# Performance work log

Measured on AMD Instinct MI355X. Metric: run time of the kernel, lower is better.

Reference implementation:

```python
import jax, jax.numpy as jnp
import numpy as np

B, N, F_IN, F_OUT = 64, 1024, 256, 64


def setup_inputs() -> dict:
    key = jax.random.key(0)
    k1, k2, k3, k4 = jax.random.split(key, 4)
    # xavier_uniform with gain=1.414 ~= sqrt(2): limit = gain*sqrt(6/(fan_in+fan_out))
    limW = 1.414 * np.sqrt(6.0 / (F_IN + F_OUT))
    lima = 1.414 * np.sqrt(6.0 / (2 * F_OUT + 1))
    return {
        "input": jax.random.normal(k1, (B, N, F_IN), dtype=jnp.float32),
        "adj": jax.random.randint(k2, (B, N, N), 0, 2, dtype=jnp.int32),
        "W": jax.random.uniform(k3, (F_IN, F_OUT), jnp.float32, -limW, limW),
        "a": jax.random.uniform(k4, (2 * F_OUT, 1), jnp.float32, -lima, lima),
    }


def reference(input, adj, W, a):
    # h = input @ W : (B, N, Fo)
    h = jnp.matmul(input, W)
    Bs, n, Fo = h.shape
    a1 = a[:Fo, 0]   # applied to the (scrambled) left block of a_input
    a2 = a[Fo:, 0]   # applied to the tiled right block

    # The original builds a_input by repeat_interleave(N, dim=2).view -> the left
    # block's row (i*N + j) holds h[b, i, (j*Fo + t)//N] for t in [0, Fo).
    # Its dot with a1 is therefore h[b, i, :] @ M[j, :] with
    #   M[j, f] = sum_{t : (j*Fo+t)//N == f} a1[t]
    idx = (jnp.arange(n)[:, None] * Fo + jnp.arange(Fo)[None, :]) // n  # (N, Fo), values in [0, Fo)
    rows = jnp.broadcast_to(jnp.arange(n)[:, None], (n, Fo))
    M = jnp.zeros((n, Fo), h.dtype).at[rows, idx].add(jnp.broadcast_to(a1, (n, Fo)))  # (N, Fo)

    e1 = jnp.einsum("bif,jf->bij", h, M)          # left-block contribution, (B, N, N)
    e2 = jnp.einsum("bjf,f->bj", h, a2)           # right block = h tiled over i, (B, N)
    # leakyrelu result is immediately overwritten by relu in the source; only relu matters
    e = jax.nn.relu(e1 + e2[:, None, :])

    neg = jnp.asarray(-9e15, e.dtype)
    attention = jax.nn.softmax(jnp.where(adj > 0, e, neg), axis=2)
    # F.dropout omitted (inference / deterministic reference)
    h_prime = jnp.matmul(attention, h)            # (B, N, Fo)
    return jax.nn.elu(h_prime)                    # concat=True branch
```

## Files before the change

### kernel.cpp

```cpp
#include <hip/hip_runtime.h>
#include <math.h>

#define B_   64
#define N_   1024
#define FIN_ 256
#define FO_  64

__global__ __launch_bounds__(256, 2) void k1_hproj(
    const float* __restrict__ input,
    const float* __restrict__ W,
    const float* __restrict__ a,
    float* __restrict__ h,
    float* __restrict__ e2)
{
    __shared__ float in_lds[128][65];
    __shared__ float W_lds[64][64];
    const int t  = threadIdx.x;
    const int tx = t & 15;
    const int ty = t >> 4;
    const int r0 = blockIdx.x * 128;

    float acc[8][4] = {};

    for (int k0 = 0; k0 < FIN_; k0 += 64) {
        #pragma unroll
        for (int it = 0; it < 8; ++it) {
            const int row = ty + it * 16;
            const int kq  = tx * 4;
            const float4 v = *reinterpret_cast<const float4*>(
                &input[(size_t)(r0 + row) * FIN_ + k0 + kq]);
            in_lds[row][kq + 0] = v.x;
            in_lds[row][kq + 1] = v.y;
            in_lds[row][kq + 2] = v.z;
            in_lds[row][kq + 3] = v.w;
        }
        #pragma unroll
        for (int it = 0; it < 4; ++it) {
            const int kk = ty + it * 16;
            *reinterpret_cast<float4*>(&W_lds[kk][tx * 4]) =
                *reinterpret_cast<const float4*>(&W[(size_t)(k0 + kk) * FO_ + tx * 4]);
        }
        __syncthreads();

        #pragma unroll 4
        for (int k = 0; k < 64; ++k) {
            float af[8];
            #pragma unroll
            for (int mi = 0; mi < 8; ++mi) af[mi] = in_lds[ty * 8 + mi][k];
            const float4 bf = *reinterpret_cast<const float4*>(&W_lds[k][tx * 4]);
            #pragma unroll
            for (int mi = 0; mi < 8; ++mi) {
                acc[mi][0] = fmaf(af[mi], bf.x, acc[mi][0]);
                acc[mi][1] = fmaf(af[mi], bf.y, acc[mi][1]);
                acc[mi][2] = fmaf(af[mi], bf.z, acc[mi][2]);
                acc[mi][3] = fmaf(af[mi], bf.w, acc[mi][3]);
            }
        }
        __syncthreads();
    }

    const float4 a2v = *reinterpret_cast<const float4*>(&a[FO_ + tx * 4]);
    #pragma unroll
    for (int mi = 0; mi < 8; ++mi) {
        const int row = r0 + ty * 8 + mi;
        float4 hv;
        hv.x = acc[mi][0]; hv.y = acc[mi][1]; hv.z = acc[mi][2]; hv.w = acc[mi][3];
        *reinterpret_cast<float4*>(&h[(size_t)row * FO_ + tx * 4]) = hv;

        float p = acc[mi][0] * a2v.x + acc[mi][1] * a2v.y +
                  acc[mi][2] * a2v.z + acc[mi][3] * a2v.w;
        p += __shfl_xor(p, 1);
        p += __shfl_xor(p, 2);
        p += __shfl_xor(p, 4);
        p += __shfl_xor(p, 8);
        if (tx == 0) e2[row] = p;
    }
}

__global__ __launch_bounds__(256, 2) void k2_attn(
    const float* __restrict__ h,
    const int*   __restrict__ adj,
    const float* __restrict__ a,
    const float* __restrict__ e2,
    float* __restrict__ out)
{
    __shared__ float h_lds[32][64];
    __shared__ float wT[32][128];
    __shared__ float c2[128][2];
    __shared__ float e2_lds[32];
    __shared__ float den_lds[128][2];

    const int t  = threadIdx.x;
    const int tx = t & 15;
    const int ty = t >> 4;
    const int b  = blockIdx.y;
    const int i0 = blockIdx.x * 128;

    float S1 = 0.f;
    #pragma unroll
    for (int f = 0; f < FO_; f += 4) {
        const float4 av = *reinterpret_cast<const float4*>(&a[f]);
        S1 += av.x + av.y + av.z + av.w;
    }

    float acc[8][4] = {};
    float denreg = 0.f;

    const int wi  = t >> 1;
    const int ws  = t & 1;
    const int jl0 = ws * 16;

    const float* hb     = h + (size_t)b * N_ * FO_;
    const int*   adjrow = adj + ((size_t)b * N_ + i0 + wi) * N_;

    for (int jt = 0; jt < N_; jt += 32) {
        #pragma unroll
        for (int it = 0; it < 2; ++it) {
            const int idx = it * 256 + t;
            const int j   = idx >> 4;
            const int fq  = (idx & 15) * 4;
            *reinterpret_cast<float4*>(&h_lds[j][fq]) =
                *reinterpret_cast<const float4*>(&hb[(size_t)(jt + j) * FO_ + fq]);
        }
        if (t < 32) e2_lds[t] = e2[(size_t)b * N_ + jt + t];
        if (t < 128) {
            const float2 hv = *reinterpret_cast<const float2*>(
                &hb[(size_t)(i0 + t) * FO_ + (jt >> 4)]);
            c2[t][0] = S1 * hv.x;
            c2[t][1] = S1 * hv.y;
        }
        __syncthreads();

        const float c0 = c2[wi][0];
        const float c1 = c2[wi][1];
        #pragma unroll
        for (int d = 0; d < 16; d += 4) {
            const int4 av = *reinterpret_cast<const int4*>(&adjrow[jt + jl0 + d]);
            const int aa[4] = { av.x, av.y, av.z, av.w };
            #pragma unroll
            for (int dd = 0; dd < 4; ++dd) {
                const int jl = jl0 + d + dd;
                const float cg = (jl & 16) ? c1 : c0;
                const float ev = fmaxf(cg + e2_lds[jl], 0.f);
                const float w  = aa[dd] ? __expf(ev) : 0.f;
                denreg += w;
                wT[jl][wi] = w;
            }
        }
        __syncthreads();

        #pragma unroll 4
        for (int jl = 0; jl < 32; ++jl) {
            const float4 w0 = *reinterpret_cast<const float4*>(&wT[jl][ty * 8]);
            const float4 w1 = *reinterpret_cast<const float4*>(&wT[jl][ty * 8 + 4]);
            const float4 hv = *reinterpret_cast<const float4*>(&h_lds[jl][tx * 4]);
            acc[0][0] = fmaf(w0.x, hv.x, acc[0][0]); acc[0][1] = fmaf(w0.x, hv.y, acc[0][1]);
            acc[0][2] = fmaf(w0.x, hv.z, acc[0][2]); acc[0][3] = fmaf(w0.x, hv.w, acc[0][3]);
            acc[1][0] = fmaf(w0.y, hv.x, acc[1][0]); acc[1][1] = fmaf(w0.y, hv.y, acc[1][1]);
            acc[1][2] = fmaf(w0.y, hv.z, acc[1][2]); acc[1][3] = fmaf(w0.y, hv.w, acc[1][3]);
            acc[2][0] = fmaf(w0.z, hv.x, acc[2][0]); acc[2][1] = fmaf(w0.z, hv.y, acc[2][1]);
            acc[2][2] = fmaf(w0.z, hv.z, acc[2][2]); acc[2][3] = fmaf(w0.z, hv.w, acc[2][3]);
            acc[3][0] = fmaf(w0.w, hv.x, acc[3][0]); acc[3][1] = fmaf(w0.w, hv.y, acc[3][1]);
            acc[3][2] = fmaf(w0.w, hv.z, acc[3][2]); acc[3][3] = fmaf(w0.w, hv.w, acc[3][3]);
            acc[4][0] = fmaf(w1.x, hv.x, acc[4][0]); acc[4][1] = fmaf(w1.x, hv.y, acc[4][1]);
            acc[4][2] = fmaf(w1.x, hv.z, acc[4][2]); acc[4][3] = fmaf(w1.x, hv.w, acc[4][3]);
            acc[5][0] = fmaf(w1.y, hv.x, acc[5][0]); acc[5][1] = fmaf(w1.y, hv.y, acc[5][1]);
            acc[5][2] = fmaf(w1.y, hv.z, acc[5][2]); acc[5][3] = fmaf(w1.y, hv.w, acc[5][3]);
            acc[6][0] = fmaf(w1.z, hv.x, acc[6][0]); acc[6][1] = fmaf(w1.z, hv.y, acc[6][1]);
            acc[6][2] = fmaf(w1.z, hv.z, acc[6][2]); acc[6][3] = fmaf(w1.z, hv.w, acc[6][3]);
            acc[7][0] = fmaf(w1.w, hv.x, acc[7][0]); acc[7][1] = fmaf(w1.w, hv.y, acc[7][1]);
            acc[7][2] = fmaf(w1.w, hv.z, acc[7][2]); acc[7][3] = fmaf(w1.w, hv.w, acc[7][3]);
        }
        __syncthreads();
    }

    den_lds[wi][ws] = denreg;
    __syncthreads();

    #pragma unroll
    for (int mi = 0; mi < 8; ++mi) {
        const int i = ty * 8 + mi;
        const float den = den_lds[i][0] + den_lds[i][1];
        const float inv = 1.0f / den;
        float v[4];
        #pragma unroll
        for (int q = 0; q < 4; ++q) {
            const float x = acc[mi][q] * inv;
            v[q] = (x > 0.f) ? x : expm1f(x);
        }
        float4 o; o.x = v[0]; o.y = v[1]; o.z = v[2]; o.w = v[3];
        *reinterpret_cast<float4*>(
            &out[((size_t)b * N_ + i0 + i) * FO_ + tx * 4]) = o;
    }
}

extern "C" void kernel_launch(void* const* d_in, const int* in_sizes, int n_in,
                              void* d_out, int out_size, void* d_ws, size_t ws_size,
                              hipStream_t stream) {
    const float* input = (const float*)d_in[0];
    const int*   adj   = (const int*)d_in[1];
    const float* W     = (const float*)d_in[2];
    const float* a     = (const float*)d_in[3];
    float* out = (float*)d_out;

    float* h  = (float*)d_ws;
    float* e2 = (float*)((char*)d_ws + (size_t)B_ * N_ * FO_ * sizeof(float));

    k1_hproj<<<dim3((B_ * N_) / 128), dim3(256), 0, stream>>>(input, W, a, h, e2);
    k2_attn<<<dim3(N_ / 128, B_), dim3(256), 0, stream>>>(h, adj, a, e2, out);
}
```

Before: 514.3 us.

## Halve row tiles and add register-prefetch double buffering in both kernels

Both kernels now process 64 rows per block instead of 128, which doubles the grid and raises the launch-bound occupancy target to 4 blocks per CU. Global loads of the next tile (input/W in the projection, adj/h/e2 in the attention kernel) are prefetched into registers while the current tile is computed. The attention kernel double-buffers its LDS tiles so one barrier per tile replaces two. This aims to hide the latency of the memory-bound adj stream, at the cost of more register pressure and more reloads of h per batch.

```diff
diff --git a/kernel.cpp b/kernel.cpp
--- a/kernel.cpp
+++ b/kernel.cpp
@@ -6,50 +6,64 @@
 #define FIN_ 256
 #define FO_  64
 
-__global__ __launch_bounds__(256, 2) void k1_hproj(
+__global__ __launch_bounds__(256, 4) void k1_hproj(
     const float* __restrict__ input,
     const float* __restrict__ W,
     const float* __restrict__ a,
     float* __restrict__ h,
     float* __restrict__ e2)
 {
-    __shared__ float in_lds[128][65];
+    __shared__ float in_lds[64][65];
     __shared__ float W_lds[64][64];
-    const int t  = threadIdx.x;
-    const int tx = t & 15;
-    const int ty = t >> 4;
-    const int r0 = blockIdx.x * 128;
-
-    float acc[8][4] = {};
-
-    for (int k0 = 0; k0 < FIN_; k0 += 64) {
-        #pragma unroll
-        for (int it = 0; it < 8; ++it) {
-            const int row = ty + it * 16;
-            const int kq  = tx * 4;
-            const float4 v = *reinterpret_cast<const float4*>(
+
+    const int t   = threadIdx.x;
+    const int tx  = t & 15;
+    const int tyg = t >> 4;
+    const int r0  = blockIdx.x * 64;
+
+    float acc[4][4] = {};
+    float4 ireg[4], wreg[4];
+
+    auto load_chunk = [&](int k0) {
+        #pragma unroll
+        for (int it = 0; it < 4; ++it) {
+            const int idx = it * 256 + t;
+            const int row = idx >> 4;
+            const int kq  = (idx & 15) * 4;
+            ireg[it] = *reinterpret_cast<const float4*>(
                 &input[(size_t)(r0 + row) * FIN_ + k0 + kq]);
-            in_lds[row][kq + 0] = v.x;
-            in_lds[row][kq + 1] = v.y;
-            in_lds[row][kq + 2] = v.z;
-            in_lds[row][kq + 3] = v.w;
-        }
+            wreg[it] = *reinterpret_cast<const float4*>(
+                &W[(size_t)(k0 + row) * FO_ + kq]);
+        }
+    };
+    auto store_chunk = [&]() {
         #pragma unroll
         for (int it = 0; it < 4; ++it) {
-            const int kk = ty + it * 16;
-            *reinterpret_cast<float4*>(&W_lds[kk][tx * 4]) =
-                *reinterpret_cast<const float4*>(&W[(size_t)(k0 + kk) * FO_ + tx * 4]);
-        }
+            const int idx = it * 256 + t;
+            const int row = idx >> 4;
+            const int kq  = (idx & 15) * 4;
+            in_lds[row][kq + 0] = ireg[it].x;
+            in_lds[row][kq + 1] = ireg[it].y;
+            in_lds[row][kq + 2] = ireg[it].z;
+            in_lds[row][kq + 3] = ireg[it].w;
+            *reinterpret_cast<float4*>(&W_lds[row][kq]) = wreg[it];
+        }
+    };
+
+    load_chunk(0);
+    #pragma unroll 1
+    for (int c = 0; c < 4; ++c) {
+        store_chunk();
         __syncthreads();
-
+        if (c < 3) load_chunk((c + 1) * 64);
         #pragma unroll 4
         for (int k = 0; k < 64; ++k) {
-            float af[8];
+            float af[4];
             #pragma unroll
-            for (int mi = 0; mi < 8; ++mi) af[mi] = in_lds[ty * 8 + mi][k];
+            for (int mi = 0; mi < 4; ++mi) af[mi] = in_lds[tyg * 4 + mi][k];
             const float4 bf = *reinterpret_cast<const float4*>(&W_lds[k][tx * 4]);
             #pragma unroll
-            for (int mi = 0; mi < 8; ++mi) {
+            for (int mi = 0; mi < 4; ++mi) {
                 acc[mi][0] = fmaf(af[mi], bf.x, acc[mi][0]);
                 acc[mi][1] = fmaf(af[mi], bf.y, acc[mi][1]);
                 acc[mi][2] = fmaf(af[mi], bf.z, acc[mi][2]);
@@ -61,12 +75,11 @@
 
     const float4 a2v = *reinterpret_cast<const float4*>(&a[FO_ + tx * 4]);
     #pragma unroll
-    for (int mi = 0; mi < 8; ++mi) {
-        const int row = r0 + ty * 8 + mi;
+    for (int mi = 0; mi < 4; ++mi) {
+        const int row = r0 + tyg * 4 + mi;
         float4 hv;
         hv.x = acc[mi][0]; hv.y = acc[mi][1]; hv.z = acc[mi][2]; hv.w = acc[mi][3];
         *reinterpret_cast<float4*>(&h[(size_t)row * FO_ + tx * 4]) = hv;
-
         float p = acc[mi][0] * a2v.x + acc[mi][1] * a2v.y +
                   acc[mi][2] * a2v.z + acc[mi][3] * a2v.w;
         p += __shfl_xor(p, 1);
@@ -77,24 +90,30 @@
     }
 }
 
-__global__ __launch_bounds__(256, 2) void k2_attn(
+__global__ __launch_bounds__(256, 4) void k2_attn(
     const float* __restrict__ h,
     const int*   __restrict__ adj,
     const float* __restrict__ a,
     const float* __restrict__ e2,
     float* __restrict__ out)
 {
-    __shared__ float h_lds[32][64];
-    __shared__ float wT[32][128];
-    __shared__ float c2[128][2];
-    __shared__ float e2_lds[32];
-    __shared__ float den_lds[128][2];
-
-    const int t  = threadIdx.x;
-    const int tx = t & 15;
-    const int ty = t >> 4;
-    const int b  = blockIdx.y;
-    const int i0 = blockIdx.x * 128;
+    __shared__ float h_lds[2][32][64];
+    __shared__ float wT[2][32][64];
+    __shared__ float den_lds[64][4];
+
+    const int t   = threadIdx.x;
+    const int tx  = t & 15;
+    const int tyg = t >> 4;
+    const int b   = blockIdx.y;
+    const int i0  = blockIdx.x * 64;
+
+    const int wi  = t >> 2;
+    const int ws  = t & 3;
+    const int jl0 = ws * 8;
+
+    const float* hb     = h + (size_t)b * N_ * FO_;
+    const float* e2b    = e2 + (size_t)b * N_;
+    const int*   adjrow = adj + ((size_t)b * N_ + i0 + wi) * N_;
 
     float S1 = 0.f;
     #pragma unroll
@@ -103,85 +122,91 @@
         S1 += av.x + av.y + av.z + av.w;
     }
 
-    float acc[8][4] = {};
+    float acc[4][4] = {};
     float denreg = 0.f;
 
-    const int wi  = t >> 1;
-    const int ws  = t & 1;
-    const int jl0 = ws * 16;
-
-    const float* hb     = h + (size_t)b * N_ * FO_;
-    const int*   adjrow = adj + ((size_t)b * N_ + i0 + wi) * N_;
-
-    for (int jt = 0; jt < N_; jt += 32) {
+    int4   areg[2];
+    float4 hreg[2];
+    float4 e2reg[2];
+    float2 c2reg;
+
+    auto prefetch = [&](int tile) {
+        const int jt = tile * 32;
+        areg[0] = *reinterpret_cast<const int4*>(&adjrow[jt + jl0]);
+        areg[1] = *reinterpret_cast<const int4*>(&adjrow[jt + jl0 + 4]);
         #pragma unroll
         for (int it = 0; it < 2; ++it) {
             const int idx = it * 256 + t;
-            const int j   = idx >> 4;
-            const int fq  = (idx & 15) * 4;
-            *reinterpret_cast<float4*>(&h_lds[j][fq]) =
-                *reinterpret_cast<const float4*>(&hb[(size_t)(jt + j) * FO_ + fq]);
-        }
-        if (t < 32) e2_lds[t] = e2[(size_t)b * N_ + jt + t];
-        if (t < 128) {
-            const float2 hv = *reinterpret_cast<const float2*>(
-                &hb[(size_t)(i0 + t) * FO_ + (jt >> 4)]);
-            c2[t][0] = S1 * hv.x;
-            c2[t][1] = S1 * hv.y;
-        }
+            const int j = idx >> 4, fq = (idx & 15) * 4;
+            hreg[it] = *reinterpret_cast<const float4*>(
+                &hb[(size_t)(jt + j) * FO_ + fq]);
+        }
+        e2reg[0] = *reinterpret_cast<const float4*>(&e2b[jt + jl0]);
+        e2reg[1] = *reinterpret_cast<const float4*>(&e2b[jt + jl0 + 4]);
+        c2reg = *reinterpret_cast<const float2*>(
+            &hb[(size_t)(i0 + wi) * FO_ + (jt >> 4)]);
+    };
+
+    auto phaseW = [&](int buf) {
+        #pragma unroll
+        for (int it = 0; it < 2; ++it) {
+            const int idx = it * 256 + t;
+            const int j = idx >> 4, fq = (idx & 15) * 4;
+            *reinterpret_cast<float4*>(&h_lds[buf][j][fq]) = hreg[it];
+        }
+        const float cg = S1 * ((ws < 2) ? c2reg.x : c2reg.y);
+        const int   aa[8] = { areg[0].x, areg[0].y, areg[0].z, areg[0].w,
+                              areg[1].x, areg[1].y, areg[1].z, areg[1].w };
+        const float ee[8] = { e2reg[0].x, e2reg[0].y, e2reg[0].z, e2reg[0].w,
+                              e2reg[1].x, e2reg[1].y, e2reg[1].z, e2reg[1].w };
+        #pragma unroll
+        for (int dd = 0; dd < 8; ++dd) {
+            const float ev = fmaxf(cg + ee[dd], 0.f);
+            const float w  = aa[dd] ? __expf(ev) : 0.f;
+            denreg += w;
+            wT[buf][jl0 + dd][wi] = w;
+        }
+    };
+
+    auto phaseG = [&](int buf) {
+        #pragma unroll 8
+        for (int jl = 0; jl < 32; ++jl) {
+            const float4 wv = *reinterpret_cast<const float4*>(&wT[buf][jl][tyg * 4]);
+            const float4 hv = *reinterpret_cast<const float4*>(&h_lds[buf][jl][tx * 4]);
+            acc[0][0] = fmaf(wv.x, hv.x, acc[0][0]); acc[0][1] = fmaf(wv.x, hv.y, acc[0][1]);
+            acc[0][2] = fmaf(wv.x, hv.z, acc[0][2]); acc[0][3] = fmaf(wv.x, hv.w, acc[0][3]);
+            acc[1][0] = fmaf(wv.y, hv.x, acc[1][0]); acc[1][1] = fmaf(wv.y, hv.y, acc[1][1]);
+            acc[1][2] = fmaf(wv.y, hv.z, acc[1][2]); acc[1][3] = fmaf(wv.y, hv.w, acc[1][3]);
+            acc[2][0] = fmaf(wv.z, hv.x, acc[2][0]); acc[2][1] = fmaf(wv.z, hv.y, acc[2][1]);
+            acc[2][2] = fmaf(wv.z, hv.z, acc[2][2]); acc[2][3] = fmaf(wv.z, hv.w, acc[2][3]);
+            acc[3][0] = fmaf(wv.w, hv.x, acc[3][0]); acc[3][1] = fmaf(wv.w, hv.y, acc[3][1]);
+            acc[3][2] = fmaf(wv.w, hv.z, acc[3][2]); acc[3][3] = fmaf(wv.w, hv.w, acc[3][3]);
+        }
+    };
+
+    prefetch(0);
+    phaseW(0);
+    prefetch(1);
+    __syncthreads();
+
+    int cur = 0;
+    #pragma unroll 1
+    for (int tile = 0; tile < 32; ++tile) {
+        if (tile < 31) phaseW(cur ^ 1);
+        if (tile < 30) prefetch(tile + 2);
+        phaseG(cur);
         __syncthreads();
-
-        const float c0 = c2[wi][0];
-        const float c1 = c2[wi][1];
-        #pragma unroll
-        for (int d = 0; d < 16; d += 4) {
-            const int4 av = *reinterpret_cast<const int4*>(&adjrow[jt + jl0 + d]);
-            const int aa[4] = { av.x, av.y, av.z, av.w };
-            #pragma unroll
-            for (int dd = 0; dd < 4; ++dd) {
-                const int jl = jl0 + d + dd;
-                const float cg = (jl & 16) ? c1 : c0;
-                const float ev = fmaxf(cg + e2_lds[jl], 0.f);
-                const float w  = aa[dd] ? __expf(ev) : 0.f;
-                denreg += w;
-                wT[jl][wi] = w;
-            }
-        }
-        __syncthreads();
-
-        #pragma unroll 4
-        for (int jl = 0; jl < 32; ++jl) {
-            const float4 w0 = *reinterpret_cast<const float4*>(&wT[jl][ty * 8]);
-            const float4 w1 = *reinterpret_cast<const float4*>(&wT[jl][ty * 8 + 4]);
-            const float4 hv = *reinterpret_cast<const float4*>(&h_lds[jl][tx * 4]);
-            acc[0][0] = fmaf(w0.x, hv.x, acc[0][0]); acc[0][1] = fmaf(w0.x, hv.y, acc[0][1]);
-            acc[0][2] = fmaf(w0.x, hv.z, acc[0][2]); acc[0][3] = fmaf(w0.x, hv.w, acc[0][3]);
-            acc[1][0] = fmaf(w0.y, hv.x, acc[1][0]); acc[1][1] = fmaf(w0.y, hv.y, acc[1][1]);
-            acc[1][2] = fmaf(w0.y, hv.z, acc[1][2]); acc[1][3] = fmaf(w0.y, hv.w, acc[1][3]);
-            acc[2][0] = fmaf(w0.z, hv.x, acc[2][0]); acc[2][1] = fmaf(w0.z, hv.y, acc[2][1]);
-            acc[2][2] = fmaf(w0.z, hv.z, acc[2][2]); acc[2][3] = fmaf(w0.z, hv.w, acc[2][3]);
-            acc[3][0] = fmaf(w0.w, hv.x, acc[3][0]); acc[3][1] = fmaf(w0.w, hv.y, acc[3][1]);
-            acc[3][2] = fmaf(w0.w, hv.z, acc[3][2]); acc[3][3] = fmaf(w0.w, hv.w, acc[3][3]);
-            acc[4][0] = fmaf(w1.x, hv.x, acc[4][0]); acc[4][1] = fmaf(w1.x, hv.y, acc[4][1]);
-            acc[4][2] = fmaf(w1.x, hv.z, acc[4][2]); acc[4][3] = fmaf(w1.x, hv.w, acc[4][3]);
-            acc[5][0] = fmaf(w1.y, hv.x, acc[5][0]); acc[5][1] = fmaf(w1.y, hv.y, acc[5][1]);
-            acc[5][2] = fmaf(w1.y, hv.z, acc[5][2]); acc[5][3] = fmaf(w1.y, hv.w, acc[5][3]);
-            acc[6][0] = fmaf(w1.z, hv.x, acc[6][0]); acc[6][1] = fmaf(w1.z, hv.y, acc[6][1]);
-            acc[6][2] = fmaf(w1.z, hv.z, acc[6][2]); acc[6][3] = fmaf(w1.z, hv.w, acc[6][3]);
-            acc[7][0] = fmaf(w1.w, hv.x, acc[7][0]); acc[7][1] = fmaf(w1.w, hv.y, acc[7][1]);
-            acc[7][2] = fmaf(w1.w, hv.z, acc[7][2]); acc[7][3] = fmaf(w1.w, hv.w, acc[7][3]);
-        }
-        __syncthreads();
+        cur ^= 1;
     }
 
     den_lds[wi][ws] = denreg;
     __syncthreads();
 
     #pragma unroll
-    for (int mi = 0; mi < 8; ++mi) {
-        const int i = ty * 8 + mi;
-        const float den = den_lds[i][0] + den_lds[i][1];
-        const float inv = 1.0f / den;
+    for (int mi = 0; mi < 4; ++mi) {
+        const int i = tyg * 4 + mi;
+        const float4 dv = *reinterpret_cast<const float4*>(&den_lds[i][0]);
+        const float inv = 1.0f / (dv.x + dv.y + dv.z + dv.w);
         float v[4];
         #pragma unroll
         for (int q = 0; q < 4; ++q) {
@@ -206,6 +231,6 @@
     float* h  = (float*)d_ws;
     float* e2 = (float*)((char*)d_ws + (size_t)B_ * N_ * FO_ * sizeof(float));
 
-    k1_hproj<<<dim3((B_ * N_) / 128), dim3(256), 0, stream>>>(input, W, a, h, e2);
-    k2_attn<<<dim3(N_ / 128, B_), dim3(256), 0, stream>>>(h, adj, a, e2, out);
+    k1_hproj<<<dim3((B_ * N_) / 64), dim3(256), 0, stream>>>(input, W, a, h, e2);
+    k2_attn<<<dim3(N_ / 64, B_), dim3(256), 0, stream>>>(h, adj, a, e2, out);
 }
```

Result: slower. 531.2 us (+3.3%).
